# Performance work log

Measured on AMD Instinct MI355X. Metric: run time of the kernel, lower is better.

Reference implementation:

```python
import jax, jax.numpy as jnp
import numpy as np

B, N, NID, V, GH, PHI, RHO = 8, 256, 64, 128, 128, 256, 128
BN = B * N
EPS = 1e-5


def _layernorm(x, g, b):
    m = jnp.mean(x, axis=-1, keepdims=True)
    v = jnp.var(x, axis=-1, keepdims=True)
    return (x - m) * jax.lax.rsqrt(v + EPS) * g + b


def _edges(A):
    # dense adjacency -> flat batched edge list, exactly as mask.nonzero() ordering
    bidx = jnp.arange(B)[:, None, None]
    ii = jnp.arange(N)[None, :, None]
    jj = jnp.arange(N)[None, None, :]
    src = jnp.broadcast_to(bidx * N + ii, (B, N, N)).reshape(-1)  # edge_index[0] = b*N+i
    tgt = jnp.broadcast_to(bidx * N + jj, (B, N, N)).reshape(-1)  # edge_index[1] = b*N+j
    w = A.reshape(-1)
    valid = w != 0
    rel = (w > 0).astype(jnp.int32)
    return src, tgt, w, valid, rel


def _rgcn(H, src, tgt, valid, rel, Wrel, Wroot, bias):
    # torch_geometric RGCNConv: mean aggregation per relation at target + root + bias
    x_src = H[src]  # (E, d) gather
    out = H @ Wroot + bias
    for r in range(2):
        m = (valid & (rel == r)).astype(H.dtype)  # (E,)
        s = jax.ops.segment_sum(x_src * m[:, None], tgt, num_segments=BN)
        c = jax.ops.segment_sum(m, tgt, num_segments=BN)
        out = out + (s / jnp.maximum(c, 1.0)[:, None]) @ Wrel[r]
    return out


def setup_inputs() -> dict:
    key = jax.random.key(0)
    ks = jax.random.split(key, 24)
    p = lambda k, shape: jax.random.normal(k, shape, dtype=jnp.float32) * 0.02
    z = lambda *shape: jnp.zeros(shape, jnp.float32)
    return {
        "A": jax.random.normal(ks[0], (B, N, N), dtype=jnp.float32),
        "X": jax.random.normal(ks[1], (B, N, NID), dtype=jnp.float32),
        "home_mask": (jax.random.uniform(ks[2], (B, N)) > 0.5).astype(jnp.float32),
        "emb1_w": p(ks[3], (NID, V)), "emb1_b": z(V),
        "emb2_w": p(ks[4], (V, V)), "emb2_b": z(V),
        "rgcn_w_0": p(ks[5], (2, V, GH)), "rgcn_root_0": p(ks[6], (V, GH)), "rgcn_bias_0": z(GH),
        "lina_w_0": p(ks[7], (GH, GH)), "lina_b_0": z(GH),
        "linb_w_0": p(ks[8], (GH, GH)), "linb_b_0": z(GH),
        "rgcn_w_1": p(ks[9], (2, GH, GH)), "rgcn_root_1": p(ks[10], (GH, GH)), "rgcn_bias_1": z(GH),
        "lina_w_1": p(ks[11], (GH, GH)), "lina_b_1": z(GH),
        "linb_w_1": p(ks[12], (GH, GH)), "linb_b_1": z(GH),
        "norm_g": jnp.ones((GH,), jnp.float32), "norm_b": z(GH),
        "phi_w1": p(ks[13], (GH, PHI)), "phi_b1": z(PHI),
        "phi_w2": p(ks[14], (PHI, PHI)), "phi_b2": z(PHI),
        "rho_w1": p(ks[15], (PHI, RHO)), "rho_b1": z(RHO),
        "rho_w2": p(ks[16], (RHO, 1)), "rho_b2": z(1),
    }


def reference(A, X, home_mask, emb1_w, emb1_b, emb2_w, emb2_b,
              rgcn_w_0, rgcn_root_0, rgcn_bias_0, lina_w_0, lina_b_0, linb_w_0, linb_b_0,
              rgcn_w_1, rgcn_root_1, rgcn_bias_1, lina_w_1, lina_b_1, linb_w_1, linb_b_1,
              norm_g, norm_b, phi_w1, phi_b1, phi_w2, phi_b2,
              rho_w1, rho_b1, rho_w2, rho_b2):
    away_mask = 1.0 - home_mask
    H = jax.nn.relu(X @ emb1_w + emb1_b)
    H = (H @ emb2_w + emb2_b).reshape(BN, V)

    src, tgt, w, valid, rel = _edges(A)
    aw = jnp.abs(w) * valid.astype(w.dtype)  # |edge_weight|, zero for masked-out edges

    blocks = [
        (rgcn_w_0, rgcn_root_0, rgcn_bias_0, lina_w_0, lina_b_0, linb_w_0, linb_b_0),
        (rgcn_w_1, rgcn_root_1, rgcn_bias_1, lina_w_1, lina_b_1, linb_w_1, linb_b_1),
    ]
    agg = jnp.zeros_like(H)
    for (Wrel, Wroot, bias, law, lab, lbw, lbb) in blocks:
        H = H + agg
        H2 = _rgcn(H, src, tgt, valid, rel, Wrel, Wroot, bias)
        # gather-scale-scatter: agg[src] += H2[tgt] * |w|
        agg = jax.ops.segment_sum(H2[tgt] * aw[:, None], src, num_segments=BN)
        agg = jax.nn.relu(_layernorm(agg, norm_g, norm_b))  # dropout = identity (eval)
        agg = jax.nn.relu(agg @ law + lab)
        agg = agg @ lbw + lbb
    H = (H + agg).reshape(B, N, GH)

    # DeepSet phi (dropout = identity)
    h = jax.nn.relu(H @ phi_w1 + phi_b1)
    phi_out = jax.nn.relu(h @ phi_w2 + phi_b2)  # (B, N, PHI)

    home_sum = jnp.sum(phi_out * home_mask[:, :, None], axis=1)
    away_sum = jnp.sum(phi_out * away_mask[:, :, None], axis=1)

    def rho(s):
        return (jax.nn.relu(s @ rho_w1 + rho_b1) @ rho_w2 + rho_b2)[:, 0]

    out = rho(home_sum) - rho(away_sum)
    return 0.5 + 0.5 * jnp.tanh(out)  # (B,)
```

## Files before the change

### kernel.cpp

```cpp
#include <hip/hip_runtime.h>
#include <math.h>

#define NB 8
#define NN 256
#define DV 128

typedef __attribute__((address_space(1))) const void* gas1p;
typedef __attribute__((address_space(3))) void* las3p;
static __device__ __forceinline__ void gld16(const float* g, float* l) {
    __builtin_amdgcn_global_load_lds((gas1p)g, (las3p)l, 16, 0, 0);
}

__global__ __launch_bounds__(256, 2) void k_embed(const float* __restrict__ X,
        const float* __restrict__ w1, const float* __restrict__ b1,
        const float* __restrict__ w2, const float* __restrict__ b2,
        float* __restrict__ H, float* __restrict__ pools) {
    const int r0 = blockIdx.x * 4;
    const int t = threadIdx.x, q = t & 31, u = t >> 5;
    __shared__ __align__(16) float pool[12288];
    __shared__ __align__(16) float xq[256];
    __shared__ __align__(16) float h1q[512];
    float* part = pool + 8192;
    if (blockIdx.x < 16) pools[blockIdx.x * 256 + t] = 0.f;
    #pragma unroll
    for (int rnd = 0; rnd < 8; ++rnd) {
        int idx = rnd * 256 + t;
        gld16(w1 + idx * 4, &pool[idx * 4]);
    }
    if (t < 64) {
        float4 v;
        v.x = X[(size_t)(r0 + 0) * 64 + t];
        v.y = X[(size_t)(r0 + 1) * 64 + t];
        v.z = X[(size_t)(r0 + 2) * 64 + t];
        v.w = X[(size_t)(r0 + 3) * 64 + t];
        *(float4*)&xq[t * 4] = v;
    }
    __syncthreads();
    {
        float acc[16];
        #pragma unroll
        for (int i = 0; i < 16; ++i) acc[i] = 0.f;
        #pragma unroll
        for (int kk = 0; kk < 8; ++kk) {
            int k = u * 8 + kk;
            float4 w4 = *(const float4*)&pool[k * 128 + q * 4];
            float wc[4] = {w4.x, w4.y, w4.z, w4.w};
            float4 x4 = *(const float4*)&xq[k * 4];
            float xr[4] = {x4.x, x4.y, x4.z, x4.w};
            #pragma unroll
            for (int r = 0; r < 4; ++r)
                #pragma unroll
                for (int c = 0; c < 4; ++c)
                    acc[r * 4 + c] = fmaf(xr[r], wc[c], acc[r * 4 + c]);
        }
        #pragma unroll
        for (int r = 0; r < 4; ++r)
            *(float4*)&part[u * 512 + r * 128 + q * 4] =
                make_float4(acc[r*4+0], acc[r*4+1], acc[r*4+2], acc[r*4+3]);
    }
    __syncthreads();
    #pragma unroll
    for (int rnd = 0; rnd < 4; ++rnd) {
        int idx = rnd * 256 + t;
        gld16(w2 + idx * 4, &pool[idx * 4]);
    }
    if (t < 128) {
        int r = t >> 5, fq = t & 31;
        float4 s = *(const float4*)&b1[fq * 4];
        #pragma unroll
        for (int uu = 0; uu < 8; ++uu) {
            float4 p = *(const float4*)&part[uu * 512 + r * 128 + fq * 4];
            s.x += p.x; s.y += p.y; s.z += p.z; s.w += p.w;
        }
        h1q[(fq * 4 + 0) * 4 + r] = fmaxf(s.x, 0.f);
        h1q[(fq * 4 + 1) * 4 + r] = fmaxf(s.y, 0.f);
        h1q[(fq * 4 + 2) * 4 + r] = fmaxf(s.z, 0.f);
        h1q[(fq * 4 + 3) * 4 + r] = fmaxf(s.w, 0.f);
    }
    __syncthreads();
    float a2[16];
    #pragma unroll
    for (int i = 0; i < 16; ++i) a2[i] = 0.f;
    #pragma unroll 1
    for (int kt = 0; kt < 4; ++kt) {
        const int buf = kt & 1;
        if (kt < 3) {
            #pragma unroll
            for (int rnd = 0; rnd < 4; ++rnd) {
                int idx = rnd * 256 + t;
                gld16(w2 + (kt + 1) * 4096 + idx * 4,
                      &pool[(buf ^ 1) * 4096 + idx * 4]);
            }
        }
        const float* wt = &pool[buf * 4096];
        #pragma unroll
        for (int kk = 0; kk < 4; ++kk) {
            int kl = u * 4 + kk;
            float4 w4 = *(const float4*)&wt[kl * 128 + q * 4];
            float wc[4] = {w4.x, w4.y, w4.z, w4.w};
            float4 h4 = *(const float4*)&h1q[(kt * 32 + kl) * 4];
            float hr[4] = {h4.x, h4.y, h4.z, h4.w};
            #pragma unroll
            for (int r = 0; r < 4; ++r)
                #pragma unroll
                for (int c = 0; c < 4; ++c)
                    a2[r * 4 + c] = fmaf(hr[r], wc[c], a2[r * 4 + c]);
        }
        __syncthreads();
    }
    #pragma unroll
    for (int r = 0; r < 4; ++r)
        *(float4*)&part[u * 512 + r * 128 + q * 4] =
            make_float4(a2[r*4+0], a2[r*4+1], a2[r*4+2], a2[r*4+3]);
    __syncthreads();
    if (t < 128) {
        int r = t >> 5, fq = t & 31;
        float4 s = *(const float4*)&b2[fq * 4];
        #pragma unroll
        for (int uu = 0; uu < 8; ++uu) {
            float4 p = *(const float4*)&part[uu * 512 + r * 128 + fq * 4];
            s.x += p.x; s.y += p.y; s.z += p.z; s.w += p.w;
        }
        *(float4*)&H[(size_t)(r0 + r) * 128 + fq * 4] = s;
    }
}

__global__ __launch_bounds__(256, 2) void k_gcn1(
        const float* __restrict__ A, const float* __restrict__ H,
        const float* __restrict__ Wrel, const float* __restrict__ Wroot,
        const float* __restrict__ bias, float* __restrict__ H2) {
    const int b  = blockIdx.x >> 6;
    const int j0 = (blockIdx.x & 63) * 4;
    const int t = threadIdx.x, q = t & 31, u = t >> 5;
    __shared__ __align__(16) float pool[12288];
    __shared__ __align__(16) float pb[1536];
    __shared__ float cntp[256];
    __shared__ float cnt[8];
    float* htile = pool;
    float* maskM = pool + 8192;
    float* part  = pool;
    const float* Ab = A + (size_t)b * 65536;
    const float* Hb = H + (size_t)b * 32768;
    const float* W0 = Wrel;
    const float* W1 = Wrel + 16384;

    #pragma unroll
    for (int rnd = 0; rnd < 4; ++rnd) {
        int idx = rnd * 256 + t;
        gld16(Hb + idx * 4, &htile[idx * 4]);
    }
    {
        float4 a = *(const float4*)(Ab + (size_t)t * 256 + j0);
        float4 m0, m1;
        m0.x = (a.x < 0.f) ? 1.f : 0.f; m1.x = (a.x > 0.f) ? 1.f : 0.f;
        m0.y = (a.y < 0.f) ? 1.f : 0.f; m1.y = (a.y > 0.f) ? 1.f : 0.f;
        m0.z = (a.z < 0.f) ? 1.f : 0.f; m1.z = (a.z > 0.f) ? 1.f : 0.f;
        m0.w = (a.w < 0.f) ? 1.f : 0.f; m1.w = (a.w > 0.f) ? 1.f : 0.f;
        *(float4*)&maskM[t * 8]     = m0;
        *(float4*)&maskM[t * 8 + 4] = m1;
    }
    __syncthreads();
    {
        int chunk = t >> 3, slot = t & 7;
        float c = 0.f;
        #pragma unroll
        for (int qq = 0; qq < 8; ++qq) c += maskM[(chunk * 8 + qq) * 8 + slot];
        cntp[slot * 32 + chunk] = c;
    }
    float acc0[16], acc1[16];
    #pragma unroll
    for (int i = 0; i < 16; ++i) { acc0[i] = 0.f; acc1[i] = 0.f; }
    #pragma unroll 1
    for (int tl = 0; tl < 8; ++tl) {
        const int buf = tl & 1;
        if (tl < 7) {
            #pragma unroll
            for (int rnd = 0; rnd < 4; ++rnd) {
                int idx = rnd * 256 + t;
                gld16(Hb + (tl + 1) * 4096 + idx * 4,
                      &htile[(buf ^ 1) * 4096 + idx * 4]);
            }
        }
        const float* hb = &htile[buf * 4096];
        #pragma unroll
        for (int ii = 0; ii < 4; ++ii) {
            int iL = u * 4 + ii;
            int i  = tl * 32 + iL;
            float4 h4 = *(const float4*)&hb[iL * 128 + q * 4];
            float hc[4] = {h4.x, h4.y, h4.z, h4.w};
            float4 m0 = *(const float4*)&maskM[i * 8];
            float4 m1 = *(const float4*)&maskM[i * 8 + 4];
            float mr0[4] = {m0.x, m0.y, m0.z, m0.w};
            float mr1[4] = {m1.x, m1.y, m1.z, m1.w};
            #pragma unroll
            for (int r = 0; r < 4; ++r)
                #pragma unroll
                for (int c = 0; c < 4; ++c) {
                    acc0[r * 4 + c] = fmaf(mr0[r], hc[c], acc0[r * 4 + c]);
                    acc1[r * 4 + c] = fmaf(mr1[r], hc[c], acc1[r * 4 + c]);
                }
        }
        __syncthreads();
    }
    #pragma unroll
    for (int r = 0; r < 4; ++r) {
        *(float4*)&part[u * 1024 + r * 128 + q * 4] =
            make_float4(acc0[r*4+0], acc0[r*4+1], acc0[r*4+2], acc0[r*4+3]);
        *(float4*)&part[u * 1024 + (4 + r) * 128 + q * 4] =
            make_float4(acc1[r*4+0], acc1[r*4+1], acc1[r*4+2], acc1[r*4+3]);
    }
    if (t < 8) {
        float s = 0.f;
        #pragma unroll
        for (int c = 0; c < 32; ++c) s += cntp[t * 32 + c];
        cnt[t] = s;
    }
    __syncthreads();
// ... 8 lines not shown
        float rc = 1.f / fmaxf(cnt[slot], 1.f);
        pb[(fq * 4 + 0) * 12 + 4 + slot] = s.x * rc;
        pb[(fq * 4 + 1) * 12 + 4 + slot] = s.y * rc;
        pb[(fq * 4 + 2) * 12 + 4 + slot] = s.z * rc;
        pb[(fq * 4 + 3) * 12 + 4 + slot] = s.w * rc;
    }
    if (t < 128) {
        int r = t >> 5, fq = t & 31;
        float4 g4 = *(const float4*)(Hb + (size_t)(j0 + r) * 128 + fq * 4);
        pb[(fq * 4 + 0) * 12 + r] = g4.x;
        pb[(fq * 4 + 1) * 12 + r] = g4.y;
        pb[(fq * 4 + 2) * 12 + r] = g4.z;
        pb[(fq * 4 + 3) * 12 + r] = g4.w;
    }
    __syncthreads();
    #pragma unroll
    for (int rnd = 0; rnd < 6; ++rnd) {
        int idx = rnd * 256 + t;
        int mat = idx >> 9, rem = idx & 511;
        const float* Wm = (mat == 0) ? Wroot : ((mat == 1) ? W0 : W1);
        gld16(Wm + rem * 4, &pool[mat * 2048 + rem * 4]);
    }
    __syncthreads();
    float bcc[16];
    #pragma unroll
    for (int i = 0; i < 16; ++i) bcc[i] = 0.f;
    #pragma unroll 1
    for (int kt = 0; kt < 8; ++kt) {
        const int buf = kt & 1;
        if (kt < 7) {
            #pragma unroll
            for (int rnd = 0; rnd < 6; ++rnd) {
                int idx = rnd * 256 + t;
                int mat = idx >> 9, rem = idx & 511;
                const float* Wm = (mat == 0) ? Wroot : ((mat == 1) ? W0 : W1);
                gld16(Wm + (kt + 1) * 2048 + rem * 4,
                      &pool[(buf ^ 1) * 6144 + mat * 2048 + rem * 4]);
            }
        }
        const float* wt = &pool[buf * 6144];
        #pragma unroll
        for (int kk = 0; kk < 2; ++kk) {
            int kl = u * 2 + kk;
            int k  = kt * 16 + kl;
            float4 wr = *(const float4*)&wt[kl * 128 + q * 4];
            float4 wa = *(const float4*)&wt[2048 + kl * 128 + q * 4];
            float4 wb = *(const float4*)&wt[4096 + kl * 128 + q * 4];
            float wrc[4] = {wr.x, wr.y, wr.z, wr.w};
            float wac[4] = {wa.x, wa.y, wa.z, wa.w};
            float wbc[4] = {wb.x, wb.y, wb.z, wb.w};
            float4 hv = *(const float4*)&pb[k * 12];
            float4 q0 = *(const float4*)&pb[k * 12 + 4];
            float4 q1 = *(const float4*)&pb[k * 12 + 8];
            float hr[4] = {hv.x, hv.y, hv.z, hv.w};
            float m0r[4] = {q0.x, q0.y, q0.z, q0.w};
            float m1r[4] = {q1.x, q1.y, q1.z, q1.w};
            #pragma unroll
            for (int r = 0; r < 4; ++r)
                #pragma unroll
                for (int c = 0; c < 4; ++c) {
                    float v = bcc[r * 4 + c];
                    v = fmaf(hr[r], wrc[c], v);
                    v = fmaf(m0r[r], wac[c], v);
                    v = fmaf(m1r[r], wbc[c], v);
                    bcc[r * 4 + c] = v;
                }
        }
        __syncthreads();
    }
    float* bpart = pool;
    #pragma unroll
    for (int r = 0; r < 4; ++r)
        *(float4*)&bpart[u * 512 + r * 128 + q * 4] =
            make_float4(bcc[r*4+0], bcc[r*4+1], bcc[r*4+2], bcc[r*4+3]);
    __syncthreads();
    if (t < 128) {
        int r = t >> 5, fq = t & 31;
        float4 s = *(const float4*)&bias[fq * 4];
        #pragma unroll
        for (int uu = 0; uu < 8; ++uu) {
            float4 p = *(const float4*)&bpart[uu * 512 + r * 128 + fq * 4];
            s.x += p.x; s.y += p.y; s.z += p.z; s.w += p.w;
        }
        *(float4*)&H2[(size_t)(b * 256 + j0 + r) * 128 + fq * 4] = s;
    }
}

__global__ __launch_bounds__(256, 2) void k_gcn2(
        const float* __restrict__ A, const float* __restrict__ H2,
        const float* __restrict__ g, const float* __restrict__ bta,
        const float* __restrict__ law, const float* __restrict__ lab,
        const float* __restrict__ lbw, const float* __restrict__ lbb,
        float* __restrict__ H) {
    const int b  = blockIdx.x >> 6;
    const int i0 = (blockIdx.x & 63) * 4;
    const int t = threadIdx.x, q = t & 31, u = t >> 5;
    __shared__ __align__(16) float pool[9216];
    __shared__ __align__(16) float xq[512];
    __shared__ __align__(16) float uq[512];
    __shared__ float red[16];
    __shared__ float mi[8];
    float* tileb = pool;
    float* absA  = pool + 8192;
    float* part  = pool;
    const float* Ab  = A + (size_t)b * 65536;
    const float* H2b = H2 + (size_t)b * 32768;

    #pragma unroll
    for (int rnd = 0; rnd < 4; ++rnd) {
        int idx = rnd * 256 + t;
        gld16(H2b + idx * 4, &tileb[idx * 4]);
    }
    {
        float4 av;
        av.x = fabsf(Ab[(size_t)(i0 + 0) * 256 + t]);
        av.y = fabsf(Ab[(size_t)(i0 + 1) * 256 + t]);
        av.z = fabsf(Ab[(size_t)(i0 + 2) * 256 + t]);
        av.w = fabsf(Ab[(size_t)(i0 + 3) * 256 + t]);
        *(float4*)&absA[t * 4] = av;
    }
    __syncthreads();
    float acc[16];
    #pragma unroll
    for (int i = 0; i < 16; ++i) acc[i] = 0.f;
    #pragma unroll 1
    for (int tl = 0; tl < 8; ++tl) {
        const int buf = tl & 1;
        if (tl < 7) {
            #pragma unroll
            for (int rnd = 0; rnd < 4; ++rnd) {
                int idx = rnd * 256 + t;
                gld16(H2b + (tl + 1) * 4096 + idx * 4,
                      &tileb[(buf ^ 1) * 4096 + idx * 4]);
            }
        }
        const float* hb = &tileb[buf * 4096];
        #pragma unroll
        for (int jj = 0; jj < 4; ++jj) {
            int jL = u * 4 + jj;
            int j  = tl * 32 + jL;
            float4 h4 = *(const float4*)&hb[jL * 128 + q * 4];
            float hc[4] = {h4.x, h4.y, h4.z, h4.w};
            float4 a4 = *(const float4*)&absA[j * 4];
            float ar[4] = {a4.x, a4.y, a4.z, a4.w};
            #pragma unroll
            for (int r = 0; r < 4; ++r)
                #pragma unroll
                for (int c = 0; c < 4; ++c)
                    acc[r * 4 + c] = fmaf(ar[r], hc[c], acc[r * 4 + c]);
        }
        __syncthreads();
    }
    #pragma unroll
    for (int r = 0; r < 4; ++r)
        *(float4*)&part[u * 512 + r * 128 + q * 4] =
            make_float4(acc[r*4+0], acc[r*4+1], acc[r*4+2], acc[r*4+3]);
    __syncthreads();
    #pragma unroll
    for (int rnd = 0; rnd < 2; ++rnd) {
        int idx = rnd * 256 + t;
        gld16(law + idx * 4, &pool[4096 + idx * 4]);
    }
    float x[4] = {0.f, 0.f, 0.f, 0.f};
    if (t < 128) {
        const int wv2 = t >> 6;
        #pragma unroll
        for (int r = 0; r < 4; ++r) {
            float s = 0.f;
            #pragma unroll
            for (int uu = 0; uu < 8; ++uu) s += part[uu * 512 + r * 128 + t];
            x[r] = s;
        }
        #pragma unroll
        for (int r = 0; r < 4; ++r) {
            float s = x[r], s2 = x[r] * x[r];
            #pragma unroll
            for (int o = 32; o > 0; o >>= 1) {
// ... 17 lines not shown
    }
    __syncthreads();
    if (t < 128) {
        float gf = g[t], bf = bta[t];
        float4 xv;
        xv.x = fmaxf((x[0] - mi[0]) * mi[1] * gf + bf, 0.f);
        xv.y = fmaxf((x[1] - mi[2]) * mi[3] * gf + bf, 0.f);
        xv.z = fmaxf((x[2] - mi[4]) * mi[5] * gf + bf, 0.f);
        xv.w = fmaxf((x[3] - mi[6]) * mi[7] * gf + bf, 0.f);
        *(float4*)&xq[t * 4] = xv;
    }
    __syncthreads();
    float u1[16];
    #pragma unroll
    for (int i = 0; i < 16; ++i) u1[i] = 0.f;
    #pragma unroll 1
    for (int kt = 0; kt < 8; ++kt) {
        const int buf = kt & 1;
        if (kt < 7) {
            #pragma unroll
            for (int rnd = 0; rnd < 2; ++rnd) {
                int idx = rnd * 256 + t;
                gld16(law + (kt + 1) * 2048 + idx * 4,
                      &pool[4096 + (buf ^ 1) * 2048 + idx * 4]);
            }
        }
        const float* wt = &pool[4096 + buf * 2048];
        #pragma unroll
        for (int kk = 0; kk < 2; ++kk) {
            int kl = u * 2 + kk;
            int k  = kt * 16 + kl;
            float4 w4 = *(const float4*)&wt[kl * 128 + q * 4];
            float wc[4] = {w4.x, w4.y, w4.z, w4.w};
            float4 x4 = *(const float4*)&xq[k * 4];
            float xr[4] = {x4.x, x4.y, x4.z, x4.w};
            #pragma unroll
            for (int r = 0; r < 4; ++r)
                #pragma unroll
                for (int c = 0; c < 4; ++c)
                    u1[r * 4 + c] = fmaf(xr[r], wc[c], u1[r * 4 + c]);
        }
        __syncthreads();
    }
    #pragma unroll
    for (int r = 0; r < 4; ++r)
        *(float4*)&part[u * 512 + r * 128 + q * 4] =
            make_float4(u1[r*4+0], u1[r*4+1], u1[r*4+2], u1[r*4+3]);
    __syncthreads();
    #pragma unroll
    for (int rnd = 0; rnd < 2; ++rnd) {
        int idx = rnd * 256 + t;
        gld16(lbw + idx * 4, &pool[4096 + idx * 4]);
    }
    if (t < 128) {
        float bb = lab[t];
        float4 uv;
        float s0 = 0.f, s1 = 0.f, s2 = 0.f, s3 = 0.f;
        #pragma unroll
        for (int uu = 0; uu < 8; ++uu) {
            s0 += part[uu * 512 + 0 * 128 + t];
            s1 += part[uu * 512 + 1 * 128 + t];
            s2 += part[uu * 512 + 2 * 128 + t];
            s3 += part[uu * 512 + 3 * 128 + t];
        }
        uv.x = fmaxf(s0 + bb, 0.f);
        uv.y = fmaxf(s1 + bb, 0.f);
        uv.z = fmaxf(s2 + bb, 0.f);
        uv.w = fmaxf(s3 + bb, 0.f);
        *(float4*)&uq[t * 4] = uv;
    }
    __syncthreads();
    float u2[16];
    #pragma unroll
    for (int i = 0; i < 16; ++i) u2[i] = 0.f;
    #pragma unroll 1
    for (int kt = 0; kt < 8; ++kt) {
        const int buf = kt & 1;
        if (kt < 7) {
            #pragma unroll
            for (int rnd = 0; rnd < 2; ++rnd) {
                int idx = rnd * 256 + t;
                gld16(lbw + (kt + 1) * 2048 + idx * 4,
                      &pool[4096 + (buf ^ 1) * 2048 + idx * 4]);
            }
        }
        const float* wt = &pool[4096 + buf * 2048];
        #pragma unroll
        for (int kk = 0; kk < 2; ++kk) {
            int kl = u * 2 + kk;
            int k  = kt * 16 + kl;
            float4 w4 = *(const float4*)&wt[kl * 128 + q * 4];
            float wc[4] = {w4.x, w4.y, w4.z, w4.w};
            float4 x4 = *(const float4*)&uq[k * 4];
            float xr[4] = {x4.x, x4.y, x4.z, x4.w};
            #pragma unroll
            for (int r = 0; r < 4; ++r)
                #pragma unroll
                for (int c = 0; c < 4; ++c)
                    u2[r * 4 + c] = fmaf(xr[r], wc[c], u2[r * 4 + c]);
        }
        __syncthreads();
    }
    #pragma unroll
    for (int r = 0; r < 4; ++r)
        *(float4*)&part[u * 512 + r * 128 + q * 4] =
            make_float4(u2[r*4+0], u2[r*4+1], u2[r*4+2], u2[r*4+3]);
    __syncthreads();
    if (t < 128) {
        int r = t >> 5, fq = t & 31;
        float4 s = *(const float4*)&lbb[fq * 4];
        #pragma unroll
        for (int uu = 0; uu < 8; ++uu) {
            float4 p = *(const float4*)&part[uu * 512 + r * 128 + fq * 4];
            s.x += p.x; s.y += p.y; s.z += p.z; s.w += p.w;
        }
        float4 hold = *(const float4*)(H + (size_t)(b * 256 + i0 + r) * 128 + fq * 4);
        s.x += hold.x; s.y += hold.y; s.z += hold.z; s.w += hold.w;
        *(float4*)&H[(size_t)(b * 256 + i0 + r) * 128 + fq * 4] = s;
    }
}

__global__ __launch_bounds__(256) void k_deepset(
        const float* __restrict__ H, const float* __restrict__ hm,
        const float* __restrict__ w1, const float* __restrict__ b1,
        const float* __restrict__ w2, const float* __restrict__ b2,
        float* __restrict__ hsum, float* __restrict__ asum) {
    const int r0 = blockIdx.x * 8;
    const int b  = blockIdx.x >> 5;
    const int t  = threadIdx.x, q = t & 63, u = t >> 6;
    __shared__ __align__(16) float wt2[2][8192];
    __shared__ __align__(16) float part[8192];
    __shared__ __align__(16) float hraw[1024];
    __shared__ __align__(16) float ph2[2048];
    __shared__ float hmv[8];
    #pragma unroll
    for (int rnd = 0; rnd < 8; ++rnd) {
        int idx = rnd * 256 + t;
        gld16(w1 + idx * 4, &wt2[0][idx * 4]);
    }
    gld16(H + (size_t)r0 * 128 + t * 4, &hraw[t * 4]);
    if (t < 8) hmv[t] = hm[r0 + t];
    __syncthreads();
    float acc[32];
    #pragma unroll
    for (int i = 0; i < 32; ++i) acc[i] = 0.f;
    #pragma unroll 1
    for (int kt = 0; kt < 4; ++kt) {
        const int buf = kt & 1;
        if (kt < 3) {
            #pragma unroll
            for (int rnd = 0; rnd < 8; ++rnd) {
                int idx = rnd * 256 + t;
                gld16(w1 + (kt + 1) * 8192 + idx * 4, &wt2[buf ^ 1][idx * 4]);
            }
        }
        const float* wt = wt2[buf];
        #pragma unroll
        for (int kk = 0; kk < 8; ++kk) {
            int kl = u * 8 + kk;
            int k  = kt * 32 + kl;
            float4 w4 = *(const float4*)&wt[kl * 256 + q * 4];
            float wc[4] = {w4.x, w4.y, w4.z, w4.w};
            float hr[8];
            #pragma unroll
            for (int r = 0; r < 8; ++r) hr[r] = hraw[r * 128 + k];
            #pragma unroll
            for (int r = 0; r < 8; ++r)
                #pragma unroll
                for (int c = 0; c < 4; ++c)
                    acc[r * 4 + c] = fmaf(hr[r], wc[c], acc[r * 4 + c]);
        }
        __syncthreads();
    }
    #pragma unroll
    for (int r = 0; r < 8; ++r)
        *(float4*)&part[u * 2048 + r * 256 + q * 4] =
            make_float4(acc[r*4+0], acc[r*4+1], acc[r*4+2], acc[r*4+3]);
    __syncthreads();
    #pragma unroll
    for (int rnd = 0; rnd < 8; ++rnd) {
        int idx = rnd * 256 + t;
        gld16(w2 + idx * 4, &wt2[0][idx * 4]);
    }
    #pragma unroll
    for (int e = 0; e < 2; ++e) {
        int idx = e * 256 + t;
        int r = idx >> 6, fq = idx & 63;
        float4 s = *(const float4*)&b1[fq * 4];
        #pragma unroll
        for (int uu = 0; uu < 4; ++uu) {
            float4 p = *(const float4*)&part[uu * 2048 + r * 256 + fq * 4];
            s.x += p.x; s.y += p.y; s.z += p.z; s.w += p.w;
        }
        s.x = fmaxf(s.x, 0.f); s.y = fmaxf(s.y, 0.f);
        s.z = fmaxf(s.z, 0.f); s.w = fmaxf(s.w, 0.f);
        *(float4*)&ph2[r * 256 + fq * 4] = s;
    }
    __syncthreads();
    float a2[32];
    #pragma unroll
    for (int i = 0; i < 32; ++i) a2[i] = 0.f;
    #pragma unroll 1
    for (int kt = 0; kt < 8; ++kt) {
        const int buf = kt & 1;
        if (kt < 7) {
            #pragma unroll
            for (int rnd = 0; rnd < 8; ++rnd) {
                int idx = rnd * 256 + t;
                gld16(w2 + (kt + 1) * 8192 + idx * 4, &wt2[buf ^ 1][idx * 4]);
            }
        }
        const float* wt = wt2[buf];
        #pragma unroll
        for (int kk = 0; kk < 8; ++kk) {
            int kl = u * 8 + kk;
            int k  = kt * 32 + kl;
            float4 w4 = *(const float4*)&wt[kl * 256 + q * 4];
            float wc[4] = {w4.x, w4.y, w4.z, w4.w};
            float pr[8];
            #pragma unroll
            for (int r = 0; r < 8; ++r) pr[r] = ph2[r * 256 + k];
            #pragma unroll
            for (int r = 0; r < 8; ++r)
                #pragma unroll
                for (int c = 0; c < 4; ++c)
                    a2[r * 4 + c] = fmaf(pr[r], wc[c], a2[r * 4 + c]);
        }
        __syncthreads();
    }
    #pragma unroll
    for (int r = 0; r < 8; ++r)
        *(float4*)&part[u * 2048 + r * 256 + q * 4] =
            make_float4(a2[r*4+0], a2[r*4+1], a2[r*4+2], a2[r*4+3]);
    __syncthreads();
    {
        float bb = b2[t];
        float hp = 0.f, sp = 0.f;
        #pragma unroll
        for (int r = 0; r < 8; ++r) {
            float s = bb;
            #pragma unroll
            for (int uu = 0; uu < 4; ++uu) s += part[uu * 2048 + r * 256 + t];
            float p = fmaxf(s, 0.f);
            sp += p;
            hp = fmaf(p, hmv[r], hp);
        }
        atomicAdd(&hsum[b * 256 + t], hp);
        atomicAdd(&asum[b * 256 + t], sp - hp);
    }
}

__global__ __launch_bounds__(256) void k_rho(const float* __restrict__ hsum,
        const float* __restrict__ asum,
        const float* __restrict__ w1, const float* __restrict__ b1,
        const float* __restrict__ w2, const float* __restrict__ b2,
        float* __restrict__ out) {
    const int bIdx = blockIdx.x;
    const int t = threadIdx.x, q = t & 31, u = t >> 5;
    __shared__ __align__(16) float pool[10240];
    __shared__ __align__(16) float sv[512];
    __shared__ float wsv[2];
    float* part = pool + 8192;
    #pragma unroll
    for (int rnd = 0; rnd < 4; ++rnd) {
        int idx = rnd * 256 + t;
        gld16(w1 + idx * 4, &pool[idx * 4]);
    }
    sv[t] = hsum[bIdx * 256 + t];
    sv[256 + t] = asum[bIdx * 256 + t];
    __syncthreads();
    float aH[4] = {0.f, 0.f, 0.f, 0.f}, aA[4] = {0.f, 0.f, 0.f, 0.f};
    #pragma unroll 1
    for (int kt = 0; kt < 8; ++kt) {
        const int buf = kt & 1;
        if (kt < 7) {
            #pragma unroll
            for (int rnd = 0; rnd < 4; ++rnd) {
                int idx = rnd * 256 + t;
                gld16(w1 + (kt + 1) * 4096 + idx * 4,
                      &pool[(buf ^ 1) * 4096 + idx * 4]);
            }
        }
        const float* wt = &pool[buf * 4096];
        #pragma unroll
        for (int kk = 0; kk < 4; ++kk) {
            int kl = u * 4 + kk;
            int k  = kt * 32 + kl;
            float4 w4 = *(const float4*)&wt[kl * 128 + q * 4];
            float sh = sv[k], sa = sv[256 + k];
            aH[0] = fmaf(sh, w4.x, aH[0]); aA[0] = fmaf(sa, w4.x, aA[0]);
            aH[1] = fmaf(sh, w4.y, aH[1]); aA[1] = fmaf(sa, w4.y, aA[1]);
            aH[2] = fmaf(sh, w4.z, aH[2]); aA[2] = fmaf(sa, w4.z, aA[2]);
            aH[3] = fmaf(sh, w4.w, aH[3]); aA[3] = fmaf(sa, w4.w, aA[3]);
        }
        __syncthreads();
    }
    *(float4*)&part[u * 256 + q * 4]       = make_float4(aH[0], aH[1], aH[2], aH[3]);
    *(float4*)&part[u * 256 + 128 + q * 4] = make_float4(aA[0], aA[1], aA[2], aA[3]);
    __syncthreads();
    if (t < 64) {
        int vec = t >> 5, fq = t & 31;
        float4 s = make_float4(0.f, 0.f, 0.f, 0.f);
        #pragma unroll
        for (int uu = 0; uu < 8; ++uu) {
            float4 p = *(const float4*)&part[uu * 256 + vec * 128 + fq * 4];
            s.x += p.x; s.y += p.y; s.z += p.z; s.w += p.w;
        }
        float4 bb = *(const float4*)&b1[fq * 4];
        float4 w2q = *(const float4*)&w2[fq * 4];
        float p = fmaxf(s.x + bb.x, 0.f) * w2q.x
// ... 41 lines not shown
    float* H    = ws;
    float* H2   = ws + 262144;
    float* hsum = ws + 524288;
    float* asum = ws + 526336;

    k_embed<<<512, 256, 0, stream>>>(X, emb1_w, emb1_b, emb2_w, emb2_b, H, hsum);

    for (int it = 0; it < 2; ++it) {
        k_gcn1<<<512, 256, 0, stream>>>(A, H, rgcn_w[it], rgcn_root[it],
                                        rgcn_bias[it], H2);
        k_gcn2<<<512, 256, 0, stream>>>(A, H2, norm_g, norm_b,
                                        lina_w[it], lina_b[it],
                                        linb_w[it], linb_b[it], H);
    }

    k_deepset<<<256, 256, 0, stream>>>(H, home_mask, phi_w1, phi_b1,
                                       phi_w2, phi_b2, hsum, asum);
    k_rho<<<NB, 256, 0, stream>>>(hsum, asum, rho_w1, rho_b1, rho_w2, rho_b2, out);
}
```

Baseline: 209.2 us.

## Replace LDS double-buffered async staging with direct global loads in all kernels

Removes the global_load_lds double-buffered staging of weights and H tiles into shared memory, with its per-tile barriers, across every kernel. Threads now read float4 values straight from global memory (through the caches), each warp covering a contiguous slice of K. This cuts LDS footprint and synchronisation, which may allow more resident blocks. k_deepset is also resplit to 4 rows per block across 512 blocks instead of 8 rows across 256. The cost is more global and L2 traffic and exposed load latency, since the same weights are re-read by every block without explicit prefetch.

```diff
diff --git a/kernel.cpp b/kernel.cpp
--- a/kernel.cpp
+++ b/kernel.cpp
@@ -2,14 +2,6 @@
 #include <math.h>
 
 #define NB 8
-#define NN 256
-#define DV 128
-
-typedef __attribute__((address_space(1))) const void* gas1p;
-typedef __attribute__((address_space(3))) void* las3p;
-static __device__ __forceinline__ void gld16(const float* g, float* l) {
-    __builtin_amdgcn_global_load_lds((gas1p)g, (las3p)l, 16, 0, 0);
-}
 
 __global__ __launch_bounds__(256, 2) void k_embed(const float* __restrict__ X,
         const float* __restrict__ w1, const float* __restrict__ b1,
@@ -17,16 +9,10 @@
         float* __restrict__ H, float* __restrict__ pools) {
     const int r0 = blockIdx.x * 4;
     const int t = threadIdx.x, q = t & 31, u = t >> 5;
-    __shared__ __align__(16) float pool[12288];
+    __shared__ __align__(16) float part[4096];
     __shared__ __align__(16) float xq[256];
     __shared__ __align__(16) float h1q[512];
-    float* part = pool + 8192;
     if (blockIdx.x < 16) pools[blockIdx.x * 256 + t] = 0.f;
-    #pragma unroll
-    for (int rnd = 0; rnd < 8; ++rnd) {
-        int idx = rnd * 256 + t;
-        gld16(w1 + idx * 4, &pool[idx * 4]);
-    }
     if (t < 64) {
         float4 v;
         v.x = X[(size_t)(r0 + 0) * 64 + t];
@@ -43,7 +29,7 @@
         #pragma unroll
         for (int kk = 0; kk < 8; ++kk) {
             int k = u * 8 + kk;
-            float4 w4 = *(const float4*)&pool[k * 128 + q * 4];
+            float4 w4 = *(const float4*)&w1[(size_t)k * 128 + q * 4];
             float wc[4] = {w4.x, w4.y, w4.z, w4.w};
             float4 x4 = *(const float4*)&xq[k * 4];
             float xr[4] = {x4.x, x4.y, x4.z, x4.w};
@@ -59,11 +45,6 @@
                 make_float4(acc[r*4+0], acc[r*4+1], acc[r*4+2], acc[r*4+3]);
     }
     __syncthreads();
-    #pragma unroll
-    for (int rnd = 0; rnd < 4; ++rnd) {
-        int idx = rnd * 256 + t;
-        gld16(w2 + idx * 4, &pool[idx * 4]);
-    }
     if (t < 128) {
         int r = t >> 5, fq = t & 31;
         float4 s = *(const float4*)&b1[fq * 4];
@@ -78,27 +59,16 @@
         h1q[(fq * 4 + 3) * 4 + r] = fmaxf(s.w, 0.f);
     }
     __syncthreads();
-    float a2[16];
-    #pragma unroll
-    for (int i = 0; i < 16; ++i) a2[i] = 0.f;
-    #pragma unroll 1
-    for (int kt = 0; kt < 4; ++kt) {
-        const int buf = kt & 1;
-        if (kt < 3) {
-            #pragma unroll
-            for (int rnd = 0; rnd < 4; ++rnd) {
-                int idx = rnd * 256 + t;
-                gld16(w2 + (kt + 1) * 4096 + idx * 4,
-                      &pool[(buf ^ 1) * 4096 + idx * 4]);
-            }
-        }
-        const float* wt = &pool[buf * 4096];
-        #pragma unroll
-        for (int kk = 0; kk < 4; ++kk) {
-            int kl = u * 4 + kk;
-            float4 w4 = *(const float4*)&wt[kl * 128 + q * 4];
+    {
+        float a2[16];
+        #pragma unroll
+        for (int i = 0; i < 16; ++i) a2[i] = 0.f;
+        #pragma unroll 8
+        for (int kk = 0; kk < 16; ++kk) {
+            int k = u * 16 + kk;
+            float4 w4 = *(const float4*)&w2[(size_t)k * 128 + q * 4];
             float wc[4] = {w4.x, w4.y, w4.z, w4.w};
-            float4 h4 = *(const float4*)&h1q[(kt * 32 + kl) * 4];
+            float4 h4 = *(const float4*)&h1q[k * 4];
             float hr[4] = {h4.x, h4.y, h4.z, h4.w};
             #pragma unroll
             for (int r = 0; r < 4; ++r)
@@ -106,12 +76,11 @@
                 for (int c = 0; c < 4; ++c)
                     a2[r * 4 + c] = fmaf(hr[r], wc[c], a2[r * 4 + c]);
         }
-        __syncthreads();
-    }
-    #pragma unroll
-    for (int r = 0; r < 4; ++r)
-        *(float4*)&part[u * 512 + r * 128 + q * 4] =
-            make_float4(a2[r*4+0], a2[r*4+1], a2[r*4+2], a2[r*4+3]);
+        #pragma unroll
+        for (int r = 0; r < 4; ++r)
+            *(float4*)&part[u * 512 + r * 128 + q * 4] =
+                make_float4(a2[r*4+0], a2[r*4+1], a2[r*4+2], a2[r*4+3]);
+    }
     __syncthreads();
     if (t < 128) {
         int r = t >> 5, fq = t & 31;
@@ -132,23 +101,16 @@
     const int b  = blockIdx.x >> 6;
     const int j0 = (blockIdx.x & 63) * 4;
     const int t = threadIdx.x, q = t & 31, u = t >> 5;
-    __shared__ __align__(16) float pool[12288];
+    __shared__ __align__(16) float maskM[2048];
+    __shared__ __align__(16) float part[8192];
     __shared__ __align__(16) float pb[1536];
     __shared__ float cntp[256];
     __shared__ float cnt[8];
-    float* htile = pool;
-    float* maskM = pool + 8192;
-    float* part  = pool;
     const float* Ab = A + (size_t)b * 65536;
     const float* Hb = H + (size_t)b * 32768;
     const float* W0 = Wrel;
     const float* W1 = Wrel + 16384;
 
-    #pragma unroll
-    for (int rnd = 0; rnd < 4; ++rnd) {
-        int idx = rnd * 256 + t;
-        gld16(Hb + idx * 4, &htile[idx * 4]);
-    }
     {
         float4 a = *(const float4*)(Ab + (size_t)t * 256 + j0);
         float4 m0, m1;
@@ -170,37 +132,22 @@
     float acc0[16], acc1[16];
     #pragma unroll
     for (int i = 0; i < 16; ++i) { acc0[i] = 0.f; acc1[i] = 0.f; }
-    #pragma unroll 1
-    for (int tl = 0; tl < 8; ++tl) {
-        const int buf = tl & 1;
-        if (tl < 7) {
-            #pragma unroll
-            for (int rnd = 0; rnd < 4; ++rnd) {
-                int idx = rnd * 256 + t;
-                gld16(Hb + (tl + 1) * 4096 + idx * 4,
-                      &htile[(buf ^ 1) * 4096 + idx * 4]);
+    #pragma unroll 8
+    for (int ii = 0; ii < 32; ++ii) {
+        int i = u * 32 + ii;
+        float4 h4 = *(const float4*)&Hb[(size_t)i * 128 + q * 4];
+        float hc[4] = {h4.x, h4.y, h4.z, h4.w};
+        float4 m0 = *(const float4*)&maskM[i * 8];
+        float4 m1 = *(const float4*)&maskM[i * 8 + 4];
+        float mr0[4] = {m0.x, m0.y, m0.z, m0.w};
+        float mr1[4] = {m1.x, m1.y, m1.z, m1.w};
+        #pragma unroll
+        for (int r = 0; r < 4; ++r)
+            #pragma unroll
+            for (int c = 0; c < 4; ++c) {
+                acc0[r * 4 + c] = fmaf(mr0[r], hc[c], acc0[r * 4 + c]);
+                acc1[r * 4 + c] = fmaf(mr1[r], hc[c], acc1[r * 4 + c]);
             }
-        }
-        const float* hb = &htile[buf * 4096];
-        #pragma unroll
-        for (int ii = 0; ii < 4; ++ii) {
-            int iL = u * 4 + ii;
-            int i  = tl * 32 + iL;
-            float4 h4 = *(const float4*)&hb[iL * 128 + q * 4];
-            float hc[4] = {h4.x, h4.y, h4.z, h4.w};
-            float4 m0 = *(const float4*)&maskM[i * 8];
-            float4 m1 = *(const float4*)&maskM[i * 8 + 4];
-            float mr0[4] = {m0.x, m0.y, m0.z, m0.w};
-            float mr1[4] = {m1.x, m1.y, m1.z, m1.w};
-            #pragma unroll
-            for (int r = 0; r < 4; ++r)
-                #pragma unroll
-                for (int c = 0; c < 4; ++c) {
-                    acc0[r * 4 + c] = fmaf(mr0[r], hc[c], acc0[r * 4 + c]);
-                    acc1[r * 4 + c] = fmaf(mr1[r], hc[c], acc1[r * 4 + c]);
-                }
-        }
-        __syncthreads();
     }
     #pragma unroll
     for (int r = 0; r < 4; ++r) {
@@ -239,64 +186,38 @@
         pb[(fq * 4 + 3) * 12 + r] = g4.w;
     }
     __syncthreads();
-    #pragma unroll
-    for (int rnd = 0; rnd < 6; ++rnd) {
-        int idx = rnd * 256 + t;
-        int mat = idx >> 9, rem = idx & 511;
-        const float* Wm = (mat == 0) ? Wroot : ((mat == 1) ? W0 : W1);
-        gld16(Wm + rem * 4, &pool[mat * 2048 + rem * 4]);
-    }
-    __syncthreads();
     float bcc[16];
     #pragma unroll
     for (int i = 0; i < 16; ++i) bcc[i] = 0.f;
-    #pragma unroll 1
-    for (int kt = 0; kt < 8; ++kt) {
-        const int buf = kt & 1;
-        if (kt < 7) {
-            #pragma unroll
-            for (int rnd = 0; rnd < 6; ++rnd) {
-                int idx = rnd * 256 + t;
-                int mat = idx >> 9, rem = idx & 511;
-                const float* Wm = (mat == 0) ? Wroot : ((mat == 1) ? W0 : W1);
-                gld16(Wm + (kt + 1) * 2048 + rem * 4,
-                      &pool[(buf ^ 1) * 6144 + mat * 2048 + rem * 4]);
+    #pragma unroll 4
+    for (int kk = 0; kk < 16; ++kk) {
+        int k = u * 16 + kk;
+        float4 wr = *(const float4*)&Wroot[(size_t)k * 128 + q * 4];
+        float4 wa = *(const float4*)&W0[(size_t)k * 128 + q * 4];
+        float4 wb = *(const float4*)&W1[(size_t)k * 128 + q * 4];
+        float wrc[4] = {wr.x, wr.y, wr.z, wr.w};
+        float wac[4] = {wa.x, wa.y, wa.z, wa.w};
+        float wbc[4] = {wb.x, wb.y, wb.z, wb.w};
+        float4 hv = *(const float4*)&pb[k * 12];
+        float4 q0 = *(const float4*)&pb[k * 12 + 4];
+        float4 q1 = *(const float4*)&pb[k * 12 + 8];
+        float hr[4] = {hv.x, hv.y, hv.z, hv.w};
+        float m0r[4] = {q0.x, q0.y, q0.z, q0.w};
+        float m1r[4] = {q1.x, q1.y, q1.z, q1.w};
+        #pragma unroll
+        for (int r = 0; r < 4; ++r)
+            #pragma unroll
+            for (int c = 0; c < 4; ++c) {
+                float v = bcc[r * 4 + c];
+                v = fmaf(hr[r], wrc[c], v);
+                v = fmaf(m0r[r], wac[c], v);
+                v = fmaf(m1r[r], wbc[c], v);
+                bcc[r * 4 + c] = v;
             }
-        }
-        const float* wt = &pool[buf * 6144];
-        #pragma unroll
-        for (int kk = 0; kk < 2; ++kk) {
-            int kl = u * 2 + kk;
-            int k  = kt * 16 + kl;
-            float4 wr = *(const float4*)&wt[kl * 128 + q * 4];
-            float4 wa = *(const float4*)&wt[2048 + kl * 128 + q * 4];
-            float4 wb = *(const float4*)&wt[4096 + kl * 128 + q * 4];
-            float wrc[4] = {wr.x, wr.y, wr.z, wr.w};
-            float wac[4] = {wa.x, wa.y, wa.z, wa.w};
-            float wbc[4] = {wb.x, wb.y, wb.z, wb.w};
-            float4 hv = *(const float4*)&pb[k * 12];
-            float4 q0 = *(const float4*)&pb[k * 12 + 4];
-            float4 q1 = *(const float4*)&pb[k * 12 + 8];
-            float hr[4] = {hv.x, hv.y, hv.z, hv.w};
-            float m0r[4] = {q0.x, q0.y, q0.z, q0.w};
-            float m1r[4] = {q1.x, q1.y, q1.z, q1.w};
-            #pragma unroll
-            for (int r = 0; r < 4; ++r)
-                #pragma unroll
-                for (int c = 0; c < 4; ++c) {
-                    float v = bcc[r * 4 + c];
-                    v = fmaf(hr[r], wrc[c], v);
-                    v = fmaf(m0r[r], wac[c], v);
-                    v = fmaf(m1r[r], wbc[c], v);
-                    bcc[r * 4 + c] = v;
-                }
-        }
-        __syncthreads();
-    }
-    float* bpart = pool;
+    }
     #pragma unroll
     for (int r = 0; r < 4; ++r)
-        *(float4*)&bpart[u * 512 + r * 128 + q * 4] =
+        *(float4*)&part[u * 512 + r * 128 + q * 4] =
             make_float4(bcc[r*4+0], bcc[r*4+1], bcc[r*4+2], bcc[r*4+3]);
     __syncthreads();
     if (t < 128) {
@@ -304,7 +225,7 @@
         float4 s = *(const float4*)&bias[fq * 4];
         #pragma unroll
         for (int uu = 0; uu < 8; ++uu) {
-            float4 p = *(const float4*)&bpart[uu * 512 + r * 128 + fq * 4];
+            float4 p = *(const float4*)&part[uu * 512 + r * 128 + fq * 4];
             s.x += p.x; s.y += p.y; s.z += p.z; s.w += p.w;
         }
         *(float4*)&H2[(size_t)(b * 256 + j0 + r) * 128 + fq * 4] = s;
@@ -320,22 +241,15 @@
     const int b  = blockIdx.x >> 6;
     const int i0 = (blockIdx.x & 63) * 4;
     const int t = threadIdx.x, q = t & 31, u = t >> 5;
-    __shared__ __align__(16) float pool[9216];
+    __shared__ __align__(16) float part[4096];
+    __shared__ __align__(16) float absA[1024];
     __shared__ __align__(16) float xq[512];
     __shared__ __align__(16) float uq[512];
     __shared__ float red[16];
     __shared__ float mi[8];
-    float* tileb = pool;
-    float* absA  = pool + 8192;
-    float* part  = pool;
     const float* Ab  = A + (size_t)b * 65536;
     const float* H2b = H2 + (size_t)b * 32768;
 
-    #pragma unroll
-    for (int rnd = 0; rnd < 4; ++rnd) {
-        int idx = rnd * 256 + t;
-        gld16(H2b + idx * 4, &tileb[idx * 4]);
-    }
     {
         float4 av;
         av.x = fabsf(Ab[(size_t)(i0 + 0) * 256 + t]);
@@ -348,44 +262,24 @@
     float acc[16];
     #pragma unroll
     for (int i = 0; i < 16; ++i) acc[i] = 0.f;
-    #pragma unroll 1
-    for (int tl = 0; tl < 8; ++tl) {
-        const int buf = tl & 1;
-        if (tl < 7) {
-            #pragma unroll
-            for (int rnd = 0; rnd < 4; ++rnd) {
-                int idx = rnd * 256 + t;
-                gld16(H2b + (tl + 1) * 4096 + idx * 4,
-                      &tileb[(buf ^ 1) * 4096 + idx * 4]);
-            }
-        }
-        const float* hb = &tileb[buf * 4096];
-        #pragma unroll
-        for (int jj = 0; jj < 4; ++jj) {
-            int jL = u * 4 + jj;
-            int j  = tl * 32 + jL;
-            float4 h4 = *(const float4*)&hb[jL * 128 + q * 4];
-            float hc[4] = {h4.x, h4.y, h4.z, h4.w};
-            float4 a4 = *(const float4*)&absA[j * 4];
-            float ar[4] = {a4.x, a4.y, a4.z, a4.w};
-            #pragma unroll
-            for (int r = 0; r < 4; ++r)
-                #pragma unroll
-                for (int c = 0; c < 4; ++c)
-                    acc[r * 4 + c] = fmaf(ar[r], hc[c], acc[r * 4 + c]);
-        }
-        __syncthreads();
+    #pragma unroll 8
+    for (int jj = 0; jj < 32; ++jj) {
+        int j = u * 32 + jj;
+        float4 h4 = *(const float4*)&H2b[(size_t)j * 128 + q * 4];
+        float hc[4] = {h4.x, h4.y, h4.z, h4.w};
+        float4 a4 = *(const float4*)&absA[j * 4];
+        float ar[4] = {a4.x, a4.y, a4.z, a4.w};
+        #pragma unroll
+        for (int r = 0; r < 4; ++r)
+            #pragma unroll
+            for (int c = 0; c < 4; ++c)
+                acc[r * 4 + c] = fmaf(ar[r], hc[c], acc[r * 4 + c]);
     }
     #pragma unroll
     for (int r = 0; r < 4; ++r)
         *(float4*)&part[u * 512 + r * 128 + q * 4] =
             make_float4(acc[r*4+0], acc[r*4+1], acc[r*4+2], acc[r*4+3]);
     __syncthreads();
-    #pragma unroll
-    for (int rnd = 0; rnd < 2; ++rnd) {
-        int idx = rnd * 256 + t;
-        gld16(law + idx * 4, &pool[4096 + idx * 4]);
-    }
     float x[4] = {0.f, 0.f, 0.f, 0.f};
     if (t < 128) {
         const int wv2 = t >> 6;
@@ -433,44 +327,24 @@
     float u1[16];
     #pragma unroll
     for (int i = 0; i < 16; ++i) u1[i] = 0.f;
-    #pragma unroll 1
-    for (int kt = 0; kt < 8; ++kt) {
-        const int buf = kt & 1;
-        if (kt < 7) {
-            #pragma unroll
-            for (int rnd = 0; rnd < 2; ++rnd) {
-                int idx = rnd * 256 + t;
-                gld16(law + (kt + 1) * 2048 + idx * 4,
-                      &pool[4096 + (buf ^ 1) * 2048 + idx * 4]);
-            }
-        }
-        const float* wt = &pool[4096 + buf * 2048];
-        #pragma unroll
-        for (int kk = 0; kk < 2; ++kk) {
-            int kl = u * 2 + kk;
-            int k  = kt * 16 + kl;
-            float4 w4 = *(const float4*)&wt[kl * 128 + q * 4];
-            float wc[4] = {w4.x, w4.y, w4.z, w4.w};
-            float4 x4 = *(const float4*)&xq[k * 4];
-            float xr[4] = {x4.x, x4.y, x4.z, x4.w};
-            #pragma unroll
-            for (int r = 0; r < 4; ++r)
-                #pragma unroll
-                for (int c = 0; c < 4; ++c)
-                    u1[r * 4 + c] = fmaf(xr[r], wc[c], u1[r * 4 + c]);
-        }
-        __syncthreads();
+    #pragma unroll 8
+    for (int kk = 0; kk < 16; ++kk) {
+        int k = u * 16 + kk;
+        float4 w4 = *(const float4*)&law[(size_t)k * 128 + q * 4];
+        float wc[4] = {w4.x, w4.y, w4.z, w4.w};
+        float4 x4 = *(const float4*)&xq[k * 4];
+        float xr[4] = {x4.x, x4.y, x4.z, x4.w};
+        #pragma unroll
+        for (int r = 0; r < 4; ++r)
+            #pragma unroll
+            for (int c = 0; c < 4; ++c)
+                u1[r * 4 + c] = fmaf(xr[r], wc[c], u1[r * 4 + c]);
     }
     #pragma unroll
     for (int r = 0; r < 4; ++r)
         *(float4*)&part[u * 512 + r * 128 + q * 4] =
             make_float4(u1[r*4+0], u1[r*4+1], u1[r*4+2], u1[r*4+3]);
     __syncthreads();
-    #pragma unroll
-    for (int rnd = 0; rnd < 2; ++rnd) {
-        int idx = rnd * 256 + t;
-        gld16(lbw + idx * 4, &pool[4096 + idx * 4]);
-    }
     if (t < 128) {
         float bb = lab[t];
         float4 uv;
@@ -492,33 +366,18 @@
     float u2[16];
     #pragma unroll
     for (int i = 0; i < 16; ++i) u2[i] = 0.f;
-    #pragma unroll 1
-    for (int kt = 0; kt < 8; ++kt) {
-        const int buf = kt & 1;
-        if (kt < 7) {
-            #pragma unroll
-            for (int rnd = 0; rnd < 2; ++rnd) {
-                int idx = rnd * 256 + t;
-                gld16(lbw + (kt + 1) * 2048 + idx * 4,
-                      &pool[4096 + (buf ^ 1) * 2048 + idx * 4]);
-            }
-        }
-        const float* wt = &pool[4096 + buf * 2048];
-        #pragma unroll
-        for (int kk = 0; kk < 2; ++kk) {
-            int kl = u * 2 + kk;
-            int k  = kt * 16 + kl;
-            float4 w4 = *(const float4*)&wt[kl * 128 + q * 4];
-            float wc[4] = {w4.x, w4.y, w4.z, w4.w};
-            float4 x4 = *(const float4*)&uq[k * 4];
-            float xr[4] = {x4.x, x4.y, x4.z, x4.w};
-            #pragma unroll
-            for (int r = 0; r < 4; ++r)
-                #pragma unroll
-                for (int c = 0; c < 4; ++c)
-                    u2[r * 4 + c] = fmaf(xr[r], wc[c], u2[r * 4 + c]);
-        }
-        __syncthreads();
+    #pragma unroll 8
+    for (int kk = 0; kk < 16; ++kk) {
+        int k = u * 16 + kk;
+        float4 w4 = *(const float4*)&lbw[(size_t)k * 128 + q * 4];
+        float wc[4] = {w4.x, w4.y, w4.z, w4.w};
+        float4 x4 = *(const float4*)&uq[k * 4];
+        float xr[4] = {x4.x, x4.y, x4.z, x4.w};
+        #pragma unroll
+        for (int r = 0; r < 4; ++r)
+            #pragma unroll
+            for (int c = 0; c < 4; ++c)
+                u2[r * 4 + c] = fmaf(xr[r], wc[c], u2[r * 4 + c]);
     }
     #pragma unroll
     for (int r = 0; r < 4; ++r)
@@ -539,76 +398,52 @@
     }
 }
 
-__global__ __launch_bounds__(256) void k_deepset(
+__global__ __launch_bounds__(256, 2) void k_deepset(
         const float* __restrict__ H, const float* __restrict__ hm,
         const float* __restrict__ w1, const float* __restrict__ b1,
         const float* __restrict__ w2, const float* __restrict__ b2,
         float* __restrict__ hsum, float* __restrict__ asum) {
-    const int r0 = blockIdx.x * 8;
-    const int b  = blockIdx.x >> 5;
+    const int r0 = blockIdx.x * 4;
+    const int b  = blockIdx.x >> 6;
     const int t  = threadIdx.x, q = t & 63, u = t >> 6;
-    __shared__ __align__(16) float wt2[2][8192];
-    __shared__ __align__(16) float part[8192];
-    __shared__ __align__(16) float hraw[1024];
-    __shared__ __align__(16) float ph2[2048];
-    __shared__ float hmv[8];
-    #pragma unroll
-    for (int rnd = 0; rnd < 8; ++rnd) {
-        int idx = rnd * 256 + t;
-        gld16(w1 + idx * 4, &wt2[0][idx * 4]);
-    }
-    gld16(H + (size_t)r0 * 128 + t * 4, &hraw[t * 4]);
-    if (t < 8) hmv[t] = hm[r0 + t];
-    __syncthreads();
-    float acc[32];
-    #pragma unroll
-    for (int i = 0; i < 32; ++i) acc[i] = 0.f;
-    #pragma unroll 1
-    for (int kt = 0; kt < 4; ++kt) {
-        const int buf = kt & 1;
-        if (kt < 3) {
-            #pragma unroll
-            for (int rnd = 0; rnd < 8; ++rnd) {
-                int idx = rnd * 256 + t;
-                gld16(w1 + (kt + 1) * 8192 + idx * 4, &wt2[buf ^ 1][idx * 4]);
-            }
-        }
-        const float* wt = wt2[buf];
-        #pragma unroll
-        for (int kk = 0; kk < 8; ++kk) {
-            int kl = u * 8 + kk;
-            int k  = kt * 32 + kl;
-            float4 w4 = *(const float4*)&wt[kl * 256 + q * 4];
-            float wc[4] = {w4.x, w4.y, w4.z, w4.w};
-            float hr[8];
-            #pragma unroll
-            for (int r = 0; r < 8; ++r) hr[r] = hraw[r * 128 + k];
-            #pragma unroll
-            for (int r = 0; r < 8; ++r)
-                #pragma unroll
-                for (int c = 0; c < 4; ++c)
-                    acc[r * 4 + c] = fmaf(hr[r], wc[c], acc[r * 4 + c]);
-        }
-        __syncthreads();
-    }
-    #pragma unroll
-    for (int r = 0; r < 8; ++r)
-        *(float4*)&part[u * 2048 + r * 256 + q * 4] =
+    __shared__ __align__(16) float part[4096];
+    __shared__ __align__(16) float ph2[1024];
+    __shared__ __align__(16) float hraw[512];
+    __shared__ float hmv[4];
+    if (t < 128) {
+        float4 g4 = *(const float4*)&H[(size_t)r0 * 128 + t * 4];
+        *(float4*)&hraw[t * 4] = g4;
+    }
+    if (t < 4) hmv[t] = hm[r0 + t];
+    __syncthreads();
+    float acc[16];
+    #pragma unroll
+    for (int i = 0; i < 16; ++i) acc[i] = 0.f;
+    #pragma unroll 8
+    for (int kk = 0; kk < 32; ++kk) {
+        int k = u * 32 + kk;
+        float4 w4 = *(const float4*)&w1[(size_t)k * 256 + q * 4];
+        float wc[4] = {w4.x, w4.y, w4.z, w4.w};
+        float hr[4];
+        #pragma unroll
+        for (int r = 0; r < 4; ++r) hr[r] = hraw[r * 128 + k];
+        #pragma unroll
+        for (int r = 0; r < 4; ++r)
+            #pragma unroll
+            for (int c = 0; c < 4; ++c)
+                acc[r * 4 + c] = fmaf(hr[r], wc[c], acc[r * 4 + c]);
+    }
+    #pragma unroll
+    for (int r = 0; r < 4; ++r)
+        *(float4*)&part[u * 1024 + r * 256 + q * 4] =
             make_float4(acc[r*4+0], acc[r*4+1], acc[r*4+2], acc[r*4+3]);
     __syncthreads();
-    #pragma unroll
-    for (int rnd = 0; rnd < 8; ++rnd) {
-        int idx = rnd * 256 + t;
-        gld16(w2 + idx * 4, &wt2[0][idx * 4]);
-    }
-    #pragma unroll
-    for (int e = 0; e < 2; ++e) {
-        int idx = e * 256 + t;
-        int r = idx >> 6, fq = idx & 63;
+    {
+        int r = t >> 6, fq = t & 63;
         float4 s = *(const float4*)&b1[fq * 4];
         #pragma unroll
         for (int uu = 0; uu < 4; ++uu) {
-            float4 p = *(const float4*)&part[uu * 2048 + r * 256 + fq * 4];
+            float4 p = *(const float4*)&part[uu * 1024 + r * 256 + fq * 4];
             s.x += p.x; s.y += p.y; s.z += p.z; s.w += p.w;
         }
         s.x = fmaxf(s.x, 0.f); s.y = fmaxf(s.y, 0.f);
@@ -616,50 +451,36 @@
         *(float4*)&ph2[r * 256 + fq * 4] = s;
     }
     __syncthreads();
-    float a2[32];
-    #pragma unroll
-    for (int i = 0; i < 32; ++i) a2[i] = 0.f;
-    #pragma unroll 1
-    for (int kt = 0; kt < 8; ++kt) {
-        const int buf = kt & 1;
-        if (kt < 7) {
-            #pragma unroll
-            for (int rnd = 0; rnd < 8; ++rnd) {
-                int idx = rnd * 256 + t;
-                gld16(w2 + (kt + 1) * 8192 + idx * 4, &wt2[buf ^ 1][idx * 4]);
-            }
-        }
-        const float* wt = wt2[buf];
-        #pragma unroll
-        for (int kk = 0; kk < 8; ++kk) {
-            int kl = u * 8 + kk;
-            int k  = kt * 32 + kl;
-            float4 w4 = *(const float4*)&wt[kl * 256 + q * 4];
-            float wc[4] = {w4.x, w4.y, w4.z, w4.w};
-            float pr[8];
-            #pragma unroll
-            for (int r = 0; r < 8; ++r) pr[r] = ph2[r * 256 + k];
-            #pragma unroll
-            for (int r = 0; r < 8; ++r)
-                #pragma unroll
-                for (int c = 0; c < 4; ++c)
-                    a2[r * 4 + c] = fmaf(pr[r], wc[c], a2[r * 4 + c]);
-        }
-        __syncthreads();
-    }
-    #pragma unroll
-    for (int r = 0; r < 8; ++r)
-        *(float4*)&part[u * 2048 + r * 256 + q * 4] =
+    float a2[16];
+    #pragma unroll
+    for (int i = 0; i < 16; ++i) a2[i] = 0.f;
+    #pragma unroll 8
+    for (int kk = 0; kk < 64; ++kk) {
+        int k = u * 64 + kk;
+        float4 w4 = *(const float4*)&w2[(size_t)k * 256 + q * 4];
+        float wc[4] = {w4.x, w4.y, w4.z, w4.w};
+        float pr[4];
+        #pragma unroll
+        for (int r = 0; r < 4; ++r) pr[r] = ph2[r * 256 + k];
+        #pragma unroll
+        for (int r = 0; r < 4; ++r)
+            #pragma unroll
+            for (int c = 0; c < 4; ++c)
+                a2[r * 4 + c] = fmaf(pr[r], wc[c], a2[r * 4 + c]);
+    }
+    #pragma unroll
+    for (int r = 0; r < 4; ++r)
+        *(float4*)&part[u * 1024 + r * 256 + q * 4] =
             make_float4(a2[r*4+0], a2[r*4+1], a2[r*4+2], a2[r*4+3]);
     __syncthreads();
     {
         float bb = b2[t];
         float hp = 0.f, sp = 0.f;
         #pragma unroll
-        for (int r = 0; r < 8; ++r) {
+        for (int r = 0; r < 4; ++r) {
             float s = bb;
             #pragma unroll
-            for (int uu = 0; uu < 4; ++uu) s += part[uu * 2048 + r * 256 + t];
+            for (int uu = 0; uu < 4; ++uu) s += part[uu * 1024 + r * 256 + t];
             float p = fmaxf(s, 0.f);
             sp += p;
             hp = fmaf(p, hmv[r], hp);
@@ -676,43 +497,22 @@
         float* __restrict__ out) {
     const int bIdx = blockIdx.x;
     const int t = threadIdx.x, q = t & 31, u = t >> 5;
-    __shared__ __align__(16) float pool[10240];
+    __shared__ __align__(16) float part[2048];
     __shared__ __align__(16) float sv[512];
     __shared__ float wsv[2];
-    float* part = pool + 8192;
-    #pragma unroll
-    for (int rnd = 0; rnd < 4; ++rnd) {
-        int idx = rnd * 256 + t;
-        gld16(w1 + idx * 4, &pool[idx * 4]);
-    }
     sv[t] = hsum[bIdx * 256 + t];
     sv[256 + t] = asum[bIdx * 256 + t];
     __syncthreads();
     float aH[4] = {0.f, 0.f, 0.f, 0.f}, aA[4] = {0.f, 0.f, 0.f, 0.f};
-    #pragma unroll 1
-    for (int kt = 0; kt < 8; ++kt) {
-        const int buf = kt & 1;
-        if (kt < 7) {
-            #pragma unroll
-            for (int rnd = 0; rnd < 4; ++rnd) {
-                int idx = rnd * 256 + t;
-                gld16(w1 + (kt + 1) * 4096 + idx * 4,
-                      &pool[(buf ^ 1) * 4096 + idx * 4]);
-            }
-        }
-        const float* wt = &pool[buf * 4096];
-        #pragma unroll
-        for (int kk = 0; kk < 4; ++kk) {
-            int kl = u * 4 + kk;
-            int k  = kt * 32 + kl;
-            float4 w4 = *(const float4*)&wt[kl * 128 + q * 4];
-            float sh = sv[k], sa = sv[256 + k];
-            aH[0] = fmaf(sh, w4.x, aH[0]); aA[0] = fmaf(sa, w4.x, aA[0]);
-            aH[1] = fmaf(sh, w4.y, aH[1]); aA[1] = fmaf(sa, w4.y, aA[1]);
-            aH[2] = fmaf(sh, w4.z, aH[2]); aA[2] = fmaf(sa, w4.z, aA[2]);
-            aH[3] = fmaf(sh, w4.w, aH[3]); aA[3] = fmaf(sa, w4.w, aA[3]);
-        }
-        __syncthreads();
+    #pragma unroll 8
+    for (int kk = 0; kk < 32; ++kk) {
+        int k = u * 32 + kk;
+        float4 w4 = *(const float4*)&w1[(size_t)k * 128 + q * 4];
+        float sh = sv[k], sa = sv[256 + k];
+        aH[0] = fmaf(sh, w4.x, aH[0]); aA[0] = fmaf(sa, w4.x, aA[0]);
+        aH[1] = fmaf(sh, w4.y, aH[1]); aA[1] = fmaf(sa, w4.y, aA[1]);
+        aH[2] = fmaf(sh, w4.z, aH[2]); aA[2] = fmaf(sa, w4.z, aA[2]);
+        aH[3] = fmaf(sh, w4.w, aH[3]); aA[3] = fmaf(sa, w4.w, aA[3]);
     }
     *(float4*)&part[u * 256 + q * 4]       = make_float4(aH[0], aH[1], aH[2], aH[3]);
     *(float4*)&part[u * 256 + 128 + q * 4] = make_float4(aA[0], aA[1], aA[2], aA[3]);
@@ -784,7 +584,7 @@
                                         linb_w[it], linb_b[it], H);
     }
 
-    k_deepset<<<256, 256, 0, stream>>>(H, home_mask, phi_w1, phi_b1,
+    k_deepset<<<512, 256, 0, stream>>>(H, home_mask, phi_w1, phi_b1,
                                        phi_w2, phi_b2, hsum, asum);
     k_rho<<<NB, 256, 0, stream>>>(hsum, asum, rho_w1, rho_b1, rho_w2, rho_b2, out);
 }
```

Result: faster. 195.7 us (-6.5%).
